# Kernel tuning notes

Hardware: AMD Instinct MI355X
Metric: run time of the kernel (lower is better)

Reference implementation:

```python
import jax, jax.numpy as jnp
import numpy as np

DIM = 1024
NUM_HEADS = 16
HEAD_DIM = DIM // NUM_HEADS
EPS = 1e-5


def setup_inputs() -> dict:
    key = jax.random.key(0)
    ks = jax.random.split(key, 8)
    B, N = 4, 2048
    s = 0.02
    return {
        "x1": jax.random.normal(ks[0], (B, N, DIM), jnp.float32),
        "x2": jax.random.normal(ks[1], (B, N, DIM), jnp.float32),
        "wq": jax.random.normal(ks[2], (DIM, DIM), jnp.float32) * s,
        "bq": jnp.zeros((DIM,), jnp.float32),
        "wkv": jax.random.normal(ks[3], (DIM, 2 * DIM), jnp.float32) * s,
        "bkv": jnp.zeros((2 * DIM,), jnp.float32),
        "gamma_q": jnp.ones((HEAD_DIM,), jnp.float32),
        "beta_q": jnp.zeros((HEAD_DIM,), jnp.float32),
        "gamma_k": jnp.ones((HEAD_DIM,), jnp.float32),
        "beta_k": jnp.zeros((HEAD_DIM,), jnp.float32),
    }


def _layernorm(x, gamma, beta):
    m = jnp.mean(x, axis=-1, keepdims=True)
    v = jnp.mean(jnp.square(x - m), axis=-1, keepdims=True)
    return (x - m) * jax.lax.rsqrt(v + EPS) * gamma + beta


def reference(x1, x2, wq, bq, wkv, bkv, gamma_q, beta_q, gamma_k, beta_k):
    B, N, C = x1.shape
    H, D = NUM_HEADS, C // NUM_HEADS
    q = x1 @ wq + bq                      # [B,N,C]
    kv = x2 @ wkv + bkv                   # [B,N,2C]
    k, v = kv[..., :C], kv[..., C:]
    # [B,N,C] -> [B,H,N,D]
    q = q.reshape(B, N, H, D).transpose(0, 2, 1, 3)
    k = k.reshape(B, N, H, D).transpose(0, 2, 1, 3)
    v = v.reshape(B, N, H, D).transpose(0, 2, 1, 3)
    q = _layernorm(q, gamma_q, beta_q)
    k = _layernorm(k, gamma_k, beta_k)
    scale = 1.0 / jnp.sqrt(jnp.asarray(D, x1.dtype))
    scores = jnp.einsum("bhnd,bhmd->bhnm", q, k) * scale
    attn = jax.nn.softmax(scores, axis=-1)
    out = jnp.einsum("bhnm,bhmd->bhnd", attn, v)  # [B,H,N,D]
    return out.transpose(0, 2, 1, 3).reshape(B, N, C)
```

## Files before the change

### kernel.cpp

```cpp
#include <hip/hip_runtime.h>
#include <hip/hip_bf16.h>

#define NHEADS 16
#define HDIM 64
#define BATCH 4
#define SEQ 2048
#define CDIM 1024
#define ROWS (BATCH * SEQ)
#define QSCALE (0.125f * 1.44269504088896f)

typedef __attribute__((ext_vector_type(8))) short short8;
typedef __attribute__((ext_vector_type(4))) float f32x4;
typedef __attribute__((ext_vector_type(4))) unsigned int u32x4;

__device__ inline short f2bf(float f) {
    unsigned int u = __builtin_bit_cast(unsigned int, f);
    unsigned int r = (u + 0x7fffu + ((u >> 16) & 1u)) >> 16;
    return (short)r;
}

__device__ __forceinline__ void gll16(const void* g, void* l) {
    __builtin_amdgcn_global_load_lds(
        (const __attribute__((address_space(1))) unsigned int*)g,
        (__attribute__((address_space(3))) unsigned int*)l, 16, 0, 0);
}

__device__ __forceinline__ unsigned int pack_bf2(float a, float b) {
    return __builtin_amdgcn_perm(__builtin_bit_cast(unsigned int, b),
                                 __builtin_bit_cast(unsigned int, a), 0x07060302u);
}

__global__ __launch_bounds__(256) void cvt_bf16(const float* __restrict__ src,
                                                short* __restrict__ dst, int n8) {
    int i = blockIdx.x * 256 + threadIdx.x;
    if (i < n8) {
        f32x4 a = ((const f32x4*)src)[i * 2];
        f32x4 b = ((const f32x4*)src)[i * 2 + 1];
        short8 o;
        o[0] = f2bf(a[0]); o[1] = f2bf(a[1]); o[2] = f2bf(a[2]); o[3] = f2bf(a[3]);
        o[4] = f2bf(b[0]); o[5] = f2bf(b[1]); o[6] = f2bf(b[2]); o[7] = f2bf(b[3]);
        ((short8*)dst)[i] = o;
    }
}

__global__ __launch_bounds__(256) void wtrans(const float* __restrict__ W,
                                              short* __restrict__ WT, int Nw) {
    __shared__ short T[64][72];
    const int t = threadIdx.x;
    const int n0 = blockIdx.x * 64, k0 = blockIdx.y * 64;
    const int kl = t >> 2, c4 = (t & 3) * 16;
    const float* src = W + (size_t)(k0 + kl) * Nw + n0 + c4;
    short8 s0, s1;
#pragma unroll
    for (int e = 0; e < 2; e++) {
        f32x4 u = *(const f32x4*)(src + e * 4);
        s0[e * 4 + 0] = f2bf(u[0]); s0[e * 4 + 1] = f2bf(u[1]);
        s0[e * 4 + 2] = f2bf(u[2]); s0[e * 4 + 3] = f2bf(u[3]);
        f32x4 v = *(const f32x4*)(src + 8 + e * 4);
        s1[e * 4 + 0] = f2bf(v[0]); s1[e * 4 + 1] = f2bf(v[1]);
        s1[e * 4 + 2] = f2bf(v[2]); s1[e * 4 + 3] = f2bf(v[3]);
    }
    *(short8*)&T[kl][c4] = s0;
    *(short8*)&T[kl][c4 + 8] = s1;
    __syncthreads();
#pragma unroll
    for (int pass = 0; pass < 2; pass++) {
        int n = (t >> 3) + pass * 32;
        short8 o;
#pragma unroll
        for (int e = 0; e < 8; e++) o[e] = T[(t & 7) * 8 + e][n];
        *(short8*)(WT + (size_t)(n0 + n) * 1024 + k0 + (t & 7) * 8) = o;
    }
}

__global__ __launch_bounds__(256) void gemm_q_ln(
    const short* __restrict__ A,
    const short* __restrict__ BT,
    const float* __restrict__ bias,
    const float* __restrict__ gamma,
    const float* __restrict__ beta,
    short* __restrict__ Out)
{
    __shared__ short As[128][32];
    __shared__ short Bs[128][32];

    const int tid = threadIdx.x;
    const int wave = tid >> 6, lane = tid & 63;
    const int wr = wave >> 1, wc = wave & 1;
    const int quad = lane >> 4, l15 = lane & 15;
    const int rblk = blockIdx.y, cblk = blockIdx.x;

    f32x4 acc[4][4];
#pragma unroll
    for (int i = 0; i < 4; i++)
#pragma unroll
        for (int j = 0; j < 4; j++) acc[i][j] = f32x4{0.f, 0.f, 0.f, 0.f};

    const int srow = wave * 32 + (lane >> 2);
    const int scol = (lane & 3) * 8;

    for (int k0 = 0; k0 < CDIM; k0 += 32) {
        __syncthreads();
#pragma unroll
        for (int c = 0; c < 2; c++) {
            gll16(A + (size_t)(rblk * 128 + srow + c * 16) * CDIM + k0 + scol,
                  &As[srow + c * 16][scol]);
            gll16(BT + (size_t)(cblk * 128 + srow + c * 16) * CDIM + k0 + scol,
                  &Bs[srow + c * 16][scol]);
        }
        __syncthreads();

        short8 af[4], bfr[4];
#pragma unroll
        for (int i = 0; i < 4; i++)
            af[i] = *(const short8*)&As[wr * 64 + i * 16 + l15][quad * 8];
#pragma unroll
        for (int j = 0; j < 4; j++)
            bfr[j] = *(const short8*)&Bs[wc * 64 + j * 16 + l15][quad * 8];
#pragma unroll
        for (int i = 0; i < 4; i++)
#pragma unroll
            for (int j = 0; j < 4; j++)
                acc[i][j] = __builtin_amdgcn_mfma_f32_16x16x32_bf16(af[i], bfr[j], acc[i][j], 0, 0, 0);
    }

    const int col0 = cblk * 128 + wc * 64;
    const int h = col0 >> 6;
    float bv[4], gv[4], btv[4];
#pragma unroll
    for (int j = 0; j < 4; j++) {
        int d = j * 16 + l15;
        bv[j] = bias[col0 + d];
        gv[j] = gamma[d];
        btv[j] = beta[d];
    }
#pragma unroll
    for (int i = 0; i < 4; i++) {
        int rowl = rblk * 128 + wr * 64 + i * 16 + quad * 4;
#pragma unroll
        for (int reg = 0; reg < 4; reg++) {
            float x[4], s = 0.f, s2 = 0.f;
#pragma unroll
            for (int j = 0; j < 4; j++) {
                x[j] = acc[i][j][reg] + bv[j];
                s += x[j];
                s2 += x[j] * x[j];
            }
#pragma unroll
            for (int m = 1; m < 16; m <<= 1) {
                s += __shfl_xor(s, m);
                s2 += __shfl_xor(s2, m);
            }
            float mean = s * (1.f / 64.f);
            float var = s2 * (1.f / 64.f) - mean * mean;
            float rstd = rsqrtf(var + 1e-5f);
            int r = rowl + reg;
            int b = r >> 11, n = r & (SEQ - 1);
            size_t base = (((size_t)b * NHEADS + h) * SEQ + n) * 64;
#pragma unroll
            for (int j = 0; j < 4; j++) {
                float y = ((x[j] - mean) * rstd * gv[j] + btv[j]) * QSCALE;
                Out[base + j * 16 + l15] = f2bf(y);
            }
        }
    }
}

__global__ __launch_bounds__(256) void gemm_kv(
    const short* __restrict__ A,
    const short* __restrict__ BT,
    const float* __restrict__ bias,
    const float* __restrict__ gamma,
    const float* __restrict__ beta,
    short* __restrict__ KOut,
    short* __restrict__ VT)
{
    __shared__ short As[128][32];
    __shared__ short Bs[128][32];
    __shared__ short Ts[4][64][68];

    const int tid = threadIdx.x;
    const int wave = tid >> 6, lane = tid & 63;
    const int wr = wave >> 1, wc = wave & 1;
    const int quad = lane >> 4, l15 = lane & 15;
    const int rblk = blockIdx.y, cblk = blockIdx.x;

    f32x4 acc[4][4];
#pragma unroll
    for (int i = 0; i < 4; i++)
#pragma unroll
        for (int j = 0; j < 4; j++) acc[i][j] = f32x4{0.f, 0.f, 0.f, 0.f};

    const int srow = wave * 32 + (lane >> 2);
    const int scol = (lane & 3) * 8;

    for (int k0 = 0; k0 < CDIM; k0 += 32) {
        __syncthreads();
#pragma unroll
        for (int c = 0; c < 2; c++) {
            gll16(A + (size_t)(rblk * 128 + srow + c * 16) * CDIM + k0 + scol,
                  &As[srow + c * 16][scol]);
            gll16(BT + (size_t)(cblk * 128 + srow + c * 16) * CDIM + k0 + scol,
                  &Bs[srow + c * 16][scol]);
        }
        __syncthreads();

        short8 af[4], bfr[4];
#pragma unroll
        for (int i = 0; i < 4; i++)
            af[i] = *(const short8*)&As[wr * 64 + i * 16 + l15][quad * 8];
#pragma unroll
        for (int j = 0; j < 4; j++)
            bfr[j] = *(const short8*)&Bs[wc * 64 + j * 16 + l15][quad * 8];
#pragma unroll
        for (int i = 0; i < 4; i++)
#pragma unroll
            for (int j = 0; j < 4; j++)
                acc[i][j] = __builtin_amdgcn_mfma_f32_16x16x32_bf16(af[i], bfr[j], acc[i][j], 0, 0, 0);
    }

    const int col0 = cblk * 128 + wc * 64;
    const int g = col0 >> 6;
    float bv[4];
#pragma unroll
    for (int j = 0; j < 4; j++) bv[j] = bias[col0 + j * 16 + l15];

    if (g < NHEADS) {
        const int h = g;
        float gv[4], btv[4];
#pragma unroll
        for (int j = 0; j < 4; j++) {
            int d = j * 16 + l15;
            gv[j] = gamma[d];
            btv[j] = beta[d];
        }
#pragma unroll
        for (int i = 0; i < 4; i++) {
            int rowl = rblk * 128 + wr * 64 + i * 16 + quad * 4;
#pragma unroll
            for (int reg = 0; reg < 4; reg++) {
                float x[4], s = 0.f, s2 = 0.f;
#pragma unroll
                for (int j = 0; j < 4; j++) {
                    x[j] = acc[i][j][reg] + bv[j];
                    s += x[j];
                    s2 += x[j] * x[j];
                }
#pragma unroll
                for (int m = 1; m < 16; m <<= 1) {
                    s += __shfl_xor(s, m);
                    s2 += __shfl_xor(s2, m);
                }
                float mean = s * (1.f / 64.f);
                float var = s2 * (1.f / 64.f) - mean * mean;
                float rstd = rsqrtf(var + 1e-5f);
                int r = rowl + reg;
                int b = r >> 11, n = r & (SEQ - 1);
                size_t base = (((size_t)b * NHEADS + h) * SEQ + n) * 64;
#pragma unroll
                for (int j = 0; j < 4; j++) {
                    float y = (x[j] - mean) * rstd * gv[j] + btv[j];
                    KOut[base + j * 16 + l15] = f2bf(y);
                }
            }
        }
    } else {
        const int h = g - NHEADS;
#pragma unroll
        for (int i = 0; i < 4; i++)
#pragma unroll
            for (int reg = 0; reg < 4; reg++)
#pragma unroll
                for (int j = 0; j < 4; j++)
                    Ts[wave][i * 16 + quad * 4 + reg][j * 16 + l15] =
                        f2bf(acc[i][j][reg] + bv[j]);
        const int r = rblk * 128 + wr * 64 + lane;
        const int b = r >> 11, n = r & (SEQ - 1);
        const size_t vtbase = (((size_t)b * NHEADS + h) * 64) * SEQ;
#pragma unroll
        for (int e8 = 0; e8 < 8; e8++) {
            short8 v = *(const short8*)&Ts[wave][lane][e8 * 8];
#pragma unroll
            for (int e = 0; e < 8; e++)
                VT[vtbase + (size_t)(e8 * 8 + e) * SEQ + n] = v[e];
        }
    }
}

__global__ __launch_bounds__(256) void attn_fa(
    const short* __restrict__ Q,
    const short* __restrict__ Kk,
    const short* __restrict__ VT,
    float* __restrict__ Out)
{
    __shared__ float smem[12544];

    const int tid = threadIdx.x;
    const int w = tid >> 6, lane = tid & 63;
    const int q = lane >> 4, l15 = lane & 15;
    const int bh = blockIdx.y;
    const int b = bh >> 4, h = bh & 15;
    const int qt = blockIdx.x;
    const size_t hb = (size_t)bh * SEQ * 64;
    const size_t vb = (size_t)bh * 64 * SEQ;

    short8 qf[4][2];
#pragma unroll
    for (int qc = 0; qc < 4; qc++)
#pragma unroll
        for (int dh = 0; dh < 2; dh++)
            qf[qc][dh] = *(const short8*)(Q + hb +
                (size_t)(qt * 64 + qc * 16 + l15) * 64 + dh * 32 + q * 8);

    short8 ones;
#pragma unroll
    for (int e = 0; e < 8; e++) ones[e] = (short)0x3F80;

    f32x4 o[4][4];
#pragma unroll
    for (int jd = 0; jd < 4; jd++)
#pragma unroll
        for (int qc = 0; qc < 4; qc++) o[jd][qc] = f32x4{0.f, 0.f, 0.f, 0.f};
    f32x4 osum[4];
#pragma unroll
    for (int qc = 0; qc < 4; qc++) osum[qc] = f32x4{0.f, 0.f, 0.f, 0.f};

    unsigned int* Pd = (unsigned int*)smem + w * 1280;

    const short* kbase = Kk + hb + (size_t)(w * 32 + l15) * 64 + q * 8;
    const short* vbase = VT + vb + (size_t)l15 * SEQ + w * 32 + q * 8;

    short8 kf[2][2];
#pragma unroll
    for (int kt = 0; kt < 2; kt++)
#pragma unroll
        for (int dh = 0; dh < 2; dh++)
            kf[kt][dh] = *(const short8*)(kbase + (size_t)(kt * 16) * 64 + dh * 32);

    for (int kti = 0; kti < 16; kti++) {
        short8 vf[4];
#pragma unroll
        for (int jd = 0; jd < 4; jd++)
            vf[jd] = *(const short8*)(vbase + (size_t)(jd * 16) * SEQ + kti * 128);

        f32x4 s[2][4];
#pragma unroll
        for (int kt = 0; kt < 2; kt++)
#pragma unroll
            for (int qc = 0; qc < 4; qc++) {
                f32x4 z = f32x4{0.f, 0.f, 0.f, 0.f};
                z = __builtin_amdgcn_mfma_f32_16x16x32_bf16(kf[kt][0], qf[qc][0], z, 0, 0, 0);
                z = __builtin_amdgcn_mfma_f32_16x16x32_bf16(kf[kt][1], qf[qc][1], z, 0, 0, 0);
                s[kt][qc] = z;
            }

        int knx = kti + 1 < 16 ? kti + 1 : 15;
        short8 kn[2][2];
#pragma unroll
        for (int kt = 0; kt < 2; kt++)
#pragma unroll
            for (int dh = 0; dh < 2; dh++)
                kn[kt][dh] = *(const short8*)(kbase +
                    (size_t)(knx * 128 + kt * 16) * 64 + dh * 32);

#pragma unroll
        for (int kt = 0; kt < 2; kt++)
#pragma unroll
            for (int qc = 0; qc < 4; qc++) {
                float p0 = __builtin_amdgcn_exp2f(s[kt][qc][0]);
                float p1 = __builtin_amdgcn_exp2f(s[kt][qc][1]);
                float p2 = __builtin_amdgcn_exp2f(s[kt][qc][2]);
                float p3 = __builtin_amdgcn_exp2f(s[kt][qc][3]);
                unsigned int d0 = pack_bf2(p0, p1);
                unsigned int d1 = pack_bf2(p2, p3);
                unsigned int* p = &Pd[(qc * 16 + l15) * 20 + kt * 8 + 2 * q];
                p[0] = d0;
                p[1] = d1;
            }

        short8 pf[4];
#pragma unroll
        for (int qc = 0; qc < 4; qc++) {
            u32x4 pr = *(const u32x4*)&Pd[(qc * 16 + l15) * 20 + 4 * q];
            pf[qc] = __builtin_bit_cast(short8, pr);
        }

#pragma unroll
        for (int qc = 0; qc < 4; qc++)
            osum[qc] = __builtin_amdgcn_mfma_f32_16x16x32_bf16(ones, pf[qc], osum[qc], 0, 0, 0);
#pragma unroll
        for (int jd = 0; jd < 4; jd++)
#pragma unroll
            for (int qc = 0; qc < 4; qc++)
                o[jd][qc] = __builtin_amdgcn_mfma_f32_16x16x32_bf16(vf[jd], pf[qc], o[jd][qc], 0, 0, 0);

#pragma unroll
        for (int kt = 0; kt < 2; kt++)
#pragma unroll
            for (int dh = 0; dh < 2; dh++) kf[kt][dh] = kn[kt][dh];
    }

    __syncthreads();
    float* Ored = smem;
    float* Lred = smem + 12288;
#pragma unroll
    for (int jd = 0; jd < 4; jd++) {
        if (jd == w) continue;
        int sl = w - (w > jd ? 1 : 0);
#pragma unroll
        for (int qc = 0; qc < 4; qc++)
            *(f32x4*)&Ored[(((jd * 3 + sl) * 4 + qc) * 64 + lane) * 4] = o[jd][qc];
    }
    if (q == 0) {
#pragma unroll
        for (int qc = 0; qc < 4; qc++)
            Lred[w * 64 + qc * 16 + l15] = osum[qc][0];
    }
    __syncthreads();

#pragma unroll
    for (int sl = 0; sl < 3; sl++)
#pragma unroll
        for (int qc = 0; qc < 4; qc++) {
            f32x4 t = *(const f32x4*)&Ored[(((w * 3 + sl) * 4 + qc) * 64 + lane) * 4];
            o[w][qc] += t;
        }

#pragma unroll
    for (int qc = 0; qc < 4; qc++) {
        float l = Lred[qc * 16 + l15] + Lred[64 + qc * 16 + l15] +
                  Lred[128 + qc * 16 + l15] + Lred[192 + qc * 16 + l15];
        float inv = 1.f / l;
        f32x4 r = o[w][qc] * inv;
        int row = qt * 64 + qc * 16 + l15;
        *(f32x4*)(Out + ((size_t)b * SEQ + row) * CDIM + h * 64 + w * 16 + 4 * q) = r;
    }
}

extern "C" void kernel_launch(void* const* d_in, const int* in_sizes, int n_in,
                              void* d_out, int out_size, void* d_ws, size_t ws_size,
                              hipStream_t stream) {
    const float* x1 = (const float*)d_in[0];
    const float* x2 = (const float*)d_in[1];
    const float* wq = (const float*)d_in[2];
    const float* bq = (const float*)d_in[3];
    const float* wkv = (const float*)d_in[4];
    const float* bkv = (const float*)d_in[5];
    const float* gq = (const float*)d_in[6];
    const float* btq = (const float*)d_in[7];
    const float* gk = (const float*)d_in[8];
    const float* btk = (const float*)d_in[9];
    float* out = (float*)d_out;

    short* a1 = (short*)d_ws;
    short* a2 = a1 + (size_t)ROWS * CDIM;
    short* wqT = a2 + (size_t)ROWS * CDIM;
    short* wkvT = wqT + (size_t)CDIM * CDIM;
    short* qln = wkvT + (size_t)2 * CDIM * CDIM;
    short* kln = qln + (size_t)ROWS * CDIM;
    short* vt = kln + (size_t)ROWS * CDIM;

    const int n8 = ROWS * CDIM / 8;
    cvt_bf16<<<dim3(n8 / 256), 256, 0, stream>>>(x1, a1, n8);
    cvt_bf16<<<dim3(n8 / 256), 256, 0, stream>>>(x2, a2, n8);
    wtrans<<<dim3(16, 16), 256, 0, stream>>>(wq, wqT, CDIM);
    wtrans<<<dim3(32, 16), 256, 0, stream>>>(wkv, wkvT, 2 * CDIM);

    gemm_q_ln<<<dim3(8, 64), 256, 0, stream>>>(a1, wqT, bq, gq, btq, qln);
    gemm_kv<<<dim3(16, 64), 256, 0, stream>>>(a2, wkvT, bkv, gk, btk, kln, vt);
    attn_fa<<<dim3(32, 64), 256, 0, stream>>>(qln, kln, vt, out);
}
```

Baseline: 396.5 us.

## Drop K register prefetch, fuse exp into QK loop, restructure output reduction

Loads the K fragments inside the loop instead of software-prefetching the next tile into registers, and computes exp2 and packing right after each QK MFMA, dropping the intermediate score array. The cross-wave output reduction becomes a rotating accumulate into a shared 64x68 tile with a barrier per step, followed by coalesced row-wise stores. This lowers register pressure and the LDS footprint, but exposes K load latency and adds barriers to the epilogue.

```diff
diff --git a/kernel.cpp b/kernel.cpp
--- a/kernel.cpp
+++ b/kernel.cpp
@@ -12,6 +12,7 @@
 typedef __attribute__((ext_vector_type(8))) short short8;
 typedef __attribute__((ext_vector_type(4))) float f32x4;
 typedef __attribute__((ext_vector_type(4))) unsigned int u32x4;
+typedef __attribute__((ext_vector_type(2))) unsigned int u32x2;
 
 __device__ inline short f2bf(float f) {
     unsigned int u = __builtin_bit_cast(unsigned int, f);
@@ -293,7 +294,7 @@
     const short* __restrict__ VT,
     float* __restrict__ Out)
 {
-    __shared__ float smem[12544];
+    __shared__ __align__(16) char smem_raw[20480];
 
     const int tid = threadIdx.x;
     const int w = tid >> 6, lane = tid & 63;
@@ -304,6 +305,10 @@
     const size_t hb = (size_t)bh * SEQ * 64;
     const size_t vb = (size_t)bh * 64 * SEQ;
 
+    unsigned int* Pd = (unsigned int*)smem_raw + w * 1280;
+    float* Ot = (float*)smem_raw;
+    float* Lred = (float*)smem_raw + 64 * 68;
+
     short8 qf[4][2];
 #pragma unroll
     for (int qc = 0; qc < 4; qc++)
@@ -325,25 +330,22 @@
 #pragma unroll
     for (int qc = 0; qc < 4; qc++) osum[qc] = f32x4{0.f, 0.f, 0.f, 0.f};
 
-    unsigned int* Pd = (unsigned int*)smem + w * 1280;
-
     const short* kbase = Kk + hb + (size_t)(w * 32 + l15) * 64 + q * 8;
     const short* vbase = VT + vb + (size_t)l15 * SEQ + w * 32 + q * 8;
 
-    short8 kf[2][2];
-#pragma unroll
-    for (int kt = 0; kt < 2; kt++)
-#pragma unroll
-        for (int dh = 0; dh < 2; dh++)
-            kf[kt][dh] = *(const short8*)(kbase + (size_t)(kt * 16) * 64 + dh * 32);
-
     for (int kti = 0; kti < 16; kti++) {
+        short8 kf[2][2];
+#pragma unroll
+        for (int kt = 0; kt < 2; kt++)
+#pragma unroll
+            for (int dh = 0; dh < 2; dh++)
+                kf[kt][dh] = *(const short8*)(kbase +
+                    (size_t)(kti * 128 + kt * 16) * 64 + dh * 32);
         short8 vf[4];
 #pragma unroll
         for (int jd = 0; jd < 4; jd++)
             vf[jd] = *(const short8*)(vbase + (size_t)(jd * 16) * SEQ + kti * 128);
 
-        f32x4 s[2][4];
 #pragma unroll
         for (int kt = 0; kt < 2; kt++)
 #pragma unroll
@@ -351,31 +353,10 @@
                 f32x4 z = f32x4{0.f, 0.f, 0.f, 0.f};
                 z = __builtin_amdgcn_mfma_f32_16x16x32_bf16(kf[kt][0], qf[qc][0], z, 0, 0, 0);
                 z = __builtin_amdgcn_mfma_f32_16x16x32_bf16(kf[kt][1], qf[qc][1], z, 0, 0, 0);
-                s[kt][qc] = z;
-            }
-
-        int knx = kti + 1 < 16 ? kti + 1 : 15;
-        short8 kn[2][2];
-#pragma unroll
-        for (int kt = 0; kt < 2; kt++)
-#pragma unroll
-            for (int dh = 0; dh < 2; dh++)
-                kn[kt][dh] = *(const short8*)(kbase +
-                    (size_t)(knx * 128 + kt * 16) * 64 + dh * 32);
-
-#pragma unroll
-        for (int kt = 0; kt < 2; kt++)
-#pragma unroll
-            for (int qc = 0; qc < 4; qc++) {
-                float p0 = __builtin_amdgcn_exp2f(s[kt][qc][0]);
-                float p1 = __builtin_amdgcn_exp2f(s[kt][qc][1]);
-                float p2 = __builtin_amdgcn_exp2f(s[kt][qc][2]);
-                float p3 = __builtin_amdgcn_exp2f(s[kt][qc][3]);
-                unsigned int d0 = pack_bf2(p0, p1);
-                unsigned int d1 = pack_bf2(p2, p3);
-                unsigned int* p = &Pd[(qc * 16 + l15) * 20 + kt * 8 + 2 * q];
-                p[0] = d0;
-                p[1] = d1;
+                u32x2 d2;
+                d2[0] = pack_bf2(__builtin_amdgcn_exp2f(z[0]), __builtin_amdgcn_exp2f(z[1]));
+                d2[1] = pack_bf2(__builtin_amdgcn_exp2f(z[2]), __builtin_amdgcn_exp2f(z[3]));
+                *(u32x2*)&Pd[(qc * 16 + l15) * 20 + kt * 8 + 2 * q] = d2;
             }
 
         short8 pf[4];
@@ -393,47 +374,36 @@
 #pragma unroll
             for (int qc = 0; qc < 4; qc++)
                 o[jd][qc] = __builtin_amdgcn_mfma_f32_16x16x32_bf16(vf[jd], pf[qc], o[jd][qc], 0, 0, 0);
-
-#pragma unroll
-        for (int kt = 0; kt < 2; kt++)
-#pragma unroll
-            for (int dh = 0; dh < 2; dh++) kf[kt][dh] = kn[kt][dh];
     }
 
     __syncthreads();
-    float* Ored = smem;
-    float* Lred = smem + 12288;
-#pragma unroll
-    for (int jd = 0; jd < 4; jd++) {
-        if (jd == w) continue;
-        int sl = w - (w > jd ? 1 : 0);
+#pragma unroll
+    for (int p = 0; p < 4; p++) {
+        int jd = (w + p) & 3;
 #pragma unroll
         for (int qc = 0; qc < 4; qc++)
-            *(f32x4*)&Ored[(((jd * 3 + sl) * 4 + qc) * 64 + lane) * 4] = o[jd][qc];
-    }
-    if (q == 0) {
-#pragma unroll
-        for (int qc = 0; qc < 4; qc++)
-            Lred[w * 64 + qc * 16 + l15] = osum[qc][0];
-    }
-    __syncthreads();
-
-#pragma unroll
-    for (int sl = 0; sl < 3; sl++)
-#pragma unroll
-        for (int qc = 0; qc < 4; qc++) {
-            f32x4 t = *(const f32x4*)&Ored[(((w * 3 + sl) * 4 + qc) * 64 + lane) * 4];
-            o[w][qc] += t;
-        }
-
-#pragma unroll
-    for (int qc = 0; qc < 4; qc++) {
-        float l = Lred[qc * 16 + l15] + Lred[64 + qc * 16 + l15] +
-                  Lred[128 + qc * 16 + l15] + Lred[192 + qc * 16 + l15];
-        float inv = 1.f / l;
-        f32x4 r = o[w][qc] * inv;
-        int row = qt * 64 + qc * 16 + l15;
-        *(f32x4*)(Out + ((size_t)b * SEQ + row) * CDIM + h * 64 + w * 16 + 4 * q) = r;
+#pragma unroll
+            for (int reg = 0; reg < 4; reg++) {
+                float* dst = &Ot[(qc * 16 + l15) * 68 + jd * 16 + q * 4 + reg];
+                if (p == 0) *dst = o[jd][qc][reg];
+                else        *dst += o[jd][qc][reg];
+            }
+        if (p == 0 && q == 0) {
+#pragma unroll
+            for (int qc = 0; qc < 4; qc++)
+                Lred[w * 64 + qc * 16 + l15] = osum[qc][0];
+        }
+        __syncthreads();
+    }
+
+    const int row = tid >> 2, c = tid & 3;
+    float l = Lred[row] + Lred[64 + row] + Lred[128 + row] + Lred[192 + row];
+    float inv = 1.f / l;
+    float* obase = Out + ((size_t)b * SEQ + qt * 64 + row) * CDIM + h * 64;
+#pragma unroll
+    for (int i = 0; i < 4; i++) {
+        f32x4 t = *(const f32x4*)&Ot[row * 68 + (c + 4 * i) * 4];
+        *(f32x4*)(obase + (c + 4 * i) * 4) = t * inv;
     }
 }
 
```

After: 385.2 us. 2.8% less time.
